# Kernel tuning notes

Measured on AMD Instinct MI355X. Metric: run time of the kernel, lower is better.

The kernel has to match this reference:

```python
import jax, jax.numpy as jnp
import numpy as np

H, KV, HD = 16, 8, 128           # heads, kv heads, head_dim
THETA, EPS = 1.0e6, 1e-6         # rope theta, rmsnorm eps
QMAX = 127.0                     # symmetric int8


def qdq(x):
    """Symmetric int8 fake quant-dequant along last dim (per-token / per-out-channel)."""
    s = jnp.maximum(jnp.max(jnp.abs(x), axis=-1, keepdims=True) / QMAX, 1e-8)
    q = jnp.clip(jnp.round(x / s), -QMAX, QMAX) * s
    return x + jax.lax.stop_gradient(q - x)  # STE


def rms_norm(x, w):
    v = jnp.mean(jnp.square(x.astype(jnp.float32)), axis=-1, keepdims=True)
    return (x.astype(jnp.float32) * jax.lax.rsqrt(v + EPS)).astype(x.dtype) * w


def rotate_half(x):
    x1, x2 = jnp.split(x, 2, axis=-1)
    return jnp.concatenate([-x2, x1], axis=-1)


def setup_inputs() -> dict:
    key = jax.random.key(0)
    ks = jax.random.split(key, 6)
    B, S, D = 1, 2048, 2048
    return {
        "hidden_states": jax.random.normal(ks[0], (B, S, D), jnp.float32),
        "Wq": jax.random.normal(ks[1], (H * HD, D), jnp.float32) * 0.02,
        "Wk": jax.random.normal(ks[2], (KV * HD, D), jnp.float32) * 0.02,
        "Wv": jax.random.normal(ks[3], (KV * HD, D), jnp.float32) * 0.02,
        "Wo": jax.random.normal(ks[4], (D, H * HD), jnp.float32) * 0.02,
        "q_norm_w": jnp.ones((HD,), jnp.float32),
        "k_norm_w": jnp.ones((HD,), jnp.float32),
        "position_ids": jnp.arange(S, dtype=jnp.int32)[None, :],
    }


def reference(hidden_states, Wq, Wk, Wv, Wo, q_norm_w, k_norm_w, position_ids):
    B, S, D = hidden_states.shape
    xq = qdq(hidden_states)                                  # per-token act quant (shared input)
    q = (xq @ qdq(Wq).T).reshape(B, S, H, HD).transpose(0, 2, 1, 3)   # [B,H,S,hd]
    k = (xq @ qdq(Wk).T).reshape(B, S, KV, HD).transpose(0, 2, 1, 3)  # [B,KV,S,hd]
    v = (xq @ qdq(Wv).T).reshape(B, S, KV, HD).transpose(0, 2, 1, 3)

    q = rms_norm(q, q_norm_w)
    k = rms_norm(k, k_norm_w)

    # rotary embeddings
    inv = 1.0 / (THETA ** (jnp.arange(0, HD, 2, dtype=jnp.float32) / HD))
    freqs = position_ids.astype(jnp.float32)[..., None] * inv          # [B,S,hd/2]
    emb = jnp.concatenate([freqs, freqs], axis=-1)                     # [B,S,hd]
    cos = jnp.cos(emb)[:, None].astype(q.dtype)                        # [B,1,S,hd]
    sin = jnp.sin(emb)[:, None].astype(q.dtype)
    q = q * cos + rotate_half(q) * sin
    k = k * cos + rotate_half(k) * sin

    # qkt_matmul.quant_x1 / quant_x2
    q = qdq(q)
    k = qdq(k)

    # GQA repeat
    g = H // KV
    k = jnp.repeat(k, g, axis=1)
    v = jnp.repeat(v, g, axis=1)

    scores = jnp.einsum("bhqd,bhkd->bhqk", q, k) * (HD ** -0.5)       # [B,H,S,S]
    causal = jnp.tril(jnp.ones((S, S), bool))
    scores = jnp.where(causal[None, None], scores, jnp.float32(-1e9))
    p = jax.nn.softmax(scores.astype(jnp.float32), axis=-1).astype(q.dtype)

    # pv_matmul.quant_x1 / quant_x2
    p = qdq(p)
    v = qdq(v)
    attn = jnp.einsum("bhqk,bhkd->bhqd", p, v)                        # [B,H,S,hd]
    attn = attn.transpose(0, 2, 1, 3).reshape(B, S, H * HD)
    return qdq(attn) @ qdq(Wo).T
```

## Files before the change

kernel.cpp:

```cpp
#include <hip/hip_runtime.h>
#include <math.h>

#define NH 16
#define NKV 8
#define HDIM 128
#define SEQ 2048
#define DMODEL 2048

typedef int   v4i __attribute__((ext_vector_type(4)));
typedef float v4f __attribute__((ext_vector_type(4)));
typedef _Float16 v8h __attribute__((ext_vector_type(8)));

static constexpr float SM_SCALE = 0.08838834764831843f;

#define GLOBP(p) (__attribute__((address_space(1))) void*)(p)
#define LDSP(p)  (__attribute__((address_space(3))) void*)(p)
#define ASYNC16(g, l) __builtin_amdgcn_global_load_lds(GLOBP(g), LDSP(l), 16, 0, 0)


__device__ __forceinline__ unsigned short f2h_bits(float x) {
    _Float16 h = (_Float16)x;
    return __builtin_bit_cast(unsigned short, h);
}

__global__ __launch_bounds__(256) void quant_all_k(const float* __restrict__ hidden,
        const float* __restrict__ Wq, const float* __restrict__ Wk,
        const float* __restrict__ Wv, const float* __restrict__ Wo,
        signed char* __restrict__ out, float* __restrict__ scale) {
    int p = blockIdx.x;
    int row0g = p * 16;
    const float* in; int lr0;
    if (row0g < 2048)      { in = hidden; lr0 = row0g; }
    else if (row0g < 4096) { in = Wq; lr0 = row0g - 2048; }
    else if (row0g < 5120) { in = Wk; lr0 = row0g - 4096; }
    else if (row0g < 6144) { in = Wv; lr0 = row0g - 5120; }
    else                   { in = Wo; lr0 = row0g - 6144; }
    const int cols = 2048;
    int tid = threadIdx.x;
    __shared__ float srow[16];
    int r = tid >> 4, l16 = tid & 15;
    const float4* x4 = (const float4*)(in + (size_t)(lr0 + r) * cols);
    float amax = 0.f;
    for (int c4 = l16; c4 < (cols >> 2); c4 += 16) {
        float4 v = x4[c4];
        amax = fmaxf(amax, fmaxf(fmaxf(fabsf(v.x), fabsf(v.y)),
                                 fmaxf(fabsf(v.z), fabsf(v.w))));
    }
#pragma unroll
    for (int m = 1; m <= 8; m <<= 1) amax = fmaxf(amax, __shfl_xor(amax, m));
    if (l16 == 0) {
        float s = fmaxf(amax / 127.0f, 1e-8f);
        srow[r] = s;
        scale[row0g + r] = s;
    }
    __syncthreads();
    int total = (cols >> 4) * 16;
    size_t obase = (size_t)p * 32768;
    for (int idx = tid; idx < total; idx += 256) {
        int f = idx >> 6, q = (idx >> 4) & 3, rr = idx & 15;
        const float* src = in + (size_t)(lr0 + rr) * cols + f * 64 + q * 16;
        float s = srow[rr];
        unsigned int wds[4];
#pragma unroll
        for (int g = 0; g < 4; ++g) {
            float4 v = *(const float4*)(src + g * 4);
            int b0 = (int)fminf(fmaxf(rintf(v.x / s), -127.f), 127.f);
            int b1 = (int)fminf(fmaxf(rintf(v.y / s), -127.f), 127.f);
            int b2 = (int)fminf(fmaxf(rintf(v.z / s), -127.f), 127.f);
            int b3 = (int)fminf(fmaxf(rintf(v.w / s), -127.f), 127.f);
            wds[g] = (b0 & 255) | ((b1 & 255) << 8) | ((b2 & 255) << 16) | ((b3 & 255) << 24);
        }
        *(uint4*)(out + obase + (size_t)idx * 16) =
            make_uint4(wds[0], wds[1], wds[2], wds[3]);
    }
}

__global__ __launch_bounds__(256) void row_quant_k(const float* __restrict__ in,
        signed char* __restrict__ out, float* __restrict__ scale, int cols) {
    int row0 = blockIdx.x * 16;
    int tid = threadIdx.x;
    __shared__ float srow[16];
    int r = tid >> 4, l16 = tid & 15;
    const float4* x4 = (const float4*)(in + (size_t)(row0 + r) * cols);
    float amax = 0.f;
    for (int c4 = l16; c4 < (cols >> 2); c4 += 16) {
        float4 v = x4[c4];
        amax = fmaxf(amax, fmaxf(fmaxf(fabsf(v.x), fabsf(v.y)),
                                 fmaxf(fabsf(v.z), fabsf(v.w))));
    }
#pragma unroll
    for (int m = 1; m <= 8; m <<= 1) amax = fmaxf(amax, __shfl_xor(amax, m));
    if (l16 == 0) {
        float s = fmaxf(amax / 127.0f, 1e-8f);
        srow[r] = s;
        scale[row0 + r] = s;
    }
    __syncthreads();
    int total = (cols >> 4) * 16;
    size_t obase = ((size_t)(row0 >> 4) * (cols >> 6)) << 10;
    for (int idx = tid; idx < total; idx += 256) {
        int f = idx >> 6, q = (idx >> 4) & 3, rr = idx & 15;
        const float* src = in + (size_t)(row0 + rr) * cols + f * 64 + q * 16;
        float s = srow[rr];
        unsigned int wds[4];
#pragma unroll
        for (int g = 0; g < 4; ++g) {
            float4 v = *(const float4*)(src + g * 4);
            int b0 = (int)fminf(fmaxf(rintf(v.x / s), -127.f), 127.f);
            int b1 = (int)fminf(fmaxf(rintf(v.y / s), -127.f), 127.f);
            int b2 = (int)fminf(fmaxf(rintf(v.z / s), -127.f), 127.f);
            int b3 = (int)fminf(fmaxf(rintf(v.w / s), -127.f), 127.f);
            wds[g] = (b0 & 255) | ((b1 & 255) << 8) | ((b2 & 255) << 16) | ((b3 & 255) << 24);
        }
        *(uint4*)(out + obase + (size_t)idx * 16) =
            make_uint4(wds[0], wds[1], wds[2], wds[3]);
    }
}

__global__ __launch_bounds__(256, 3) void gemm_i8_k(const signed char* __restrict__ A,
        const float* __restrict__ sa, const signed char* __restrict__ B,
        const float* __restrict__ sb, float* __restrict__ C, int M, int N, int K) {
    __shared__ __align__(16) signed char lsA[3][8192];
    __shared__ __align__(16) signed char lsB[3][8192];
    int tid = threadIdx.x;
    int w = tid >> 6, l = tid & 63;
    int wr = w >> 1, wc = w & 1;
    int lrow = l & 15;
    int m0 = blockIdx.y * 128, n0 = blockIdx.x * 128;
    int kb6 = K >> 6;
    v4i acc[4][4];
#pragma unroll
    for (int i = 0; i < 4; ++i)
#pragma unroll
        for (int j = 0; j < 4; ++j) acc[i][j] = (v4i){0, 0, 0, 0};

    auto stage = [&](int buf, int k6) {
#pragma unroll
        for (int a = 0; a < 2; ++a) {
            int f = a * 4 + w;
            ASYNC16(A + (((size_t)(((m0 >> 4) + f) * kb6 + k6)) << 10) + l * 16,
                    lsA[buf] + f * 1024);
            ASYNC16(B + (((size_t)(((n0 >> 4) + f) * kb6 + k6)) << 10) + l * 16,
                    lsB[buf] + f * 1024);
        }
    };

    stage(0, 0);
    if (kb6 > 1) {
        stage(1, 1);
        asm volatile("s_waitcnt vmcnt(4)" ::: "memory");
    } else {
        asm volatile("s_waitcnt vmcnt(0)" ::: "memory");
    }
    __builtin_amdgcn_s_barrier();
    for (int t = 0; t < kb6; ++t) {
        if (t + 2 < kb6) stage((t + 2) % 3, t + 2);
        int cur = t % 3;
        v4i af[4], bf[4];
#pragma unroll
        for (int i = 0; i < 4; ++i) af[i] = *(const v4i*)(lsA[cur] + (wr * 4 + i) * 1024 + l * 16);
#pragma unroll
        for (int j = 0; j < 4; ++j) bf[j] = *(const v4i*)(lsB[cur] + (wc * 4 + j) * 1024 + l * 16);
#pragma unroll
        for (int i = 0; i < 4; ++i)
#pragma unroll
            for (int j = 0; j < 4; ++j)
                acc[i][j] = __builtin_amdgcn_mfma_i32_16x16x64_i8(af[i], bf[j], acc[i][j], 0, 0, 0);
        if (t + 2 < kb6) asm volatile("s_waitcnt vmcnt(4)" ::: "memory");
        else             asm volatile("s_waitcnt vmcnt(0)" ::: "memory");
        __builtin_amdgcn_s_barrier();
    }
    int r0 = m0 + wr * 64, c0 = n0 + wc * 64;
    int lg = l >> 4;
    float sbv[4];
#pragma unroll
    for (int j = 0; j < 4; ++j) sbv[j] = sb[c0 + j * 16 + lrow];
#pragma unroll
    for (int i = 0; i < 4; ++i) {
        float4 s4 = *(const float4*)(sa + r0 + i * 16 + lg * 4);
        float sav[4] = {s4.x, s4.y, s4.z, s4.w};
#pragma unroll
        for (int j = 0; j < 4; ++j) {
#pragma unroll
            for (int reg = 0; reg < 4; ++reg) {
                int rr = r0 + i * 16 + lg * 4 + reg;
                C[(size_t)rr * N + c0 + j * 16 + lrow] = (float)acc[i][j][reg] * (sav[reg] * sbv[j]);
            }
        }
    }
}

__global__ __launch_bounds__(256, 2) void gemm_qkv_k(const signed char* __restrict__ A,
        const float* __restrict__ sa, const signed char* __restrict__ B,
        const float* __restrict__ sb,
        const float* __restrict__ qw, const float* __restrict__ kw,
        const float* __restrict__ ct, const float* __restrict__ st,
        signed char* __restrict__ q_i8, float* __restrict__ sq,
        signed char* __restrict__ k_i8, float* __restrict__ sk,
        unsigned short* __restrict__ vtT) {
    __shared__ __align__(16) char smem[68608];
    signed char (*lsA)[8192] = (signed char(*)[8192])smem;
    signed char (*lsB)[8192] = (signed char(*)[8192])(smem + 24576);
    float (*tile)[132] = (float(*)[132])smem;
    float* srow = (float*)(smem + 67584);
    int tid = threadIdx.x;
    int w = tid >> 6, l = tid & 63;
    int wr = w >> 1, wc = w & 1;
    int lrow = l & 15, lg = l >> 4;
    int m0 = blockIdx.y * 128, n0 = blockIdx.x * 128;
    const int kb6 = 32;
    v4i acc[4][4];
#pragma unroll
    for (int i = 0; i < 4; ++i)
#pragma unroll
        for (int j = 0; j < 4; ++j) acc[i][j] = (v4i){0, 0, 0, 0};

    auto stage = [&](int buf, int k6) {
#pragma unroll
        for (int a = 0; a < 2; ++a) {
            int f = a * 4 + w;
            ASYNC16(A + (((size_t)(((m0 >> 4) + f) * kb6 + k6)) << 10) + l * 16,
                    lsA[buf] + f * 1024);
            ASYNC16(B + (((size_t)(((n0 >> 4) + f) * kb6 + k6)) << 10) + l * 16,
                    lsB[buf] + f * 1024);
        }
    };

    stage(0, 0);
    stage(1, 1);
    asm volatile("s_waitcnt vmcnt(4)" ::: "memory");
    __builtin_amdgcn_s_barrier();
    for (int t = 0; t < kb6; ++t) {
        if (t + 2 < kb6) stage((t + 2) % 3, t + 2);
        int cur = t % 3;
        v4i af[4], bf[4];
#pragma unroll
        for (int i = 0; i < 4; ++i) af[i] = *(const v4i*)(lsA[cur] + (wr * 4 + i) * 1024 + l * 16);
#pragma unroll
        for (int j = 0; j < 4; ++j) bf[j] = *(const v4i*)(lsB[cur] + (wc * 4 + j) * 1024 + l * 16);
#pragma unroll
        for (int i = 0; i < 4; ++i)
#pragma unroll
            for (int j = 0; j < 4; ++j)
                acc[i][j] = __builtin_amdgcn_mfma_i32_16x16x64_i8(af[i], bf[j], acc[i][j], 0, 0, 0);
        if (t + 2 < kb6) asm volatile("s_waitcnt vmcnt(4)" ::: "memory");
        else             asm volatile("s_waitcnt vmcnt(0)" ::: "memory");
        __builtin_amdgcn_s_barrier();
    }
    {
        int c0 = n0 + wc * 64;
        float sbv[4];
#pragma unroll
        for (int j = 0; j < 4; ++j) sbv[j] = sb[c0 + j * 16 + lrow];
#pragma unroll
        for (int i = 0; i < 4; ++i) {
            float4 s4 = *(const float4*)(sa + m0 + wr * 64 + i * 16 + lg * 4);
            float sav[4] = {s4.x, s4.y, s4.z, s4.w};
#pragma unroll
            for (int j = 0; j < 4; ++j)
#pragma unroll
                for (int reg = 0; reg < 4; ++reg)
                    tile[wr * 64 + i * 16 + lg * 4 + reg][wc * 64 + j * 16 + lrow] =
                        (float)acc[i][j][reg] * (sav[reg] * sbv[j]);
        }
    }
    __syncthreads();
    int slot = n0 >> 7;
    if (slot < 24) {
        const float* wn = (slot < 16) ? qw : kw;
        signed char* dst8 = (slot < 16) ? q_i8 + (size_t)slot * (SEQ * 128)
                                        : k_i8 + (size_t)(slot - 16) * (SEQ * 128);
        float* sdst = (slot < 16) ? sq + (size_t)slot * SEQ : sk + (size_t)(slot - 16) * SEQ;
        float wn0 = wn[l], wn1 = wn[l + 64];
        for (int it = 0; it < 32; ++it) {
            int tl = it * 4 + w;
            int t = m0 + tl;
            float x0 = tile[tl][l];
            float x1 = tile[tl][l + 64];
            float ss = x0 * x0 + x1 * x1;
#pragma unroll
            for (int m = 1; m <= 32; m <<= 1) ss += __shfl_xor(ss, m);
            float rs = 1.0f / sqrtf(ss / 128.0f + 1e-6f);
            x0 = (x0 * rs) * wn0;
            x1 = (x1 * rs) * wn1;
            float cth = ct[t * 64 + l];
            float sth = st[t * 64 + l];
            float nx0 = x0 * cth - x1 * sth;
            float nx1 = x1 * cth + x0 * sth;
            float amax = fmaxf(fabsf(nx0), fabsf(nx1));
#pragma unroll
            for (int m = 1; m <= 32; m <<= 1) amax = fmaxf(amax, __shfl_xor(amax, m));
            float s = fmaxf(amax / 127.0f, 1e-8f);
            float q0 = fminf(fmaxf(rintf(nx0 / s), -127.f), 127.f);
            float q1 = fminf(fmaxf(rintf(nx1 / s), -127.f), 127.f);
            size_t ta0 = (size_t)(((t >> 4) * 2) << 10)
                       + (size_t)((((l >> 4) & 3) << 8) + ((t & 15) << 4) + (l & 15));
            dst8[ta0] = (signed char)(int)q0;
            dst8[ta0 + 1024] = (signed char)(int)q1;
            if (l == 0) sdst[t] = s;
        }
    } else {
        int kv = slot - 24;
        for (int it = 0; it < 32; ++it) {
            int tl = it * 4 + w;
            float x0 = tile[tl][l];
            float x1 = tile[tl][l + 64];
            float amax = fmaxf(fabsf(x0), fabsf(x1));
#pragma unroll
            for (int m = 1; m <= 32; m <<= 1) amax = fmaxf(amax, __shfl_xor(amax, m));
            if (l == 0) srow[tl] = fmaxf(amax / 127.0f, 1e-8f);
        }
        __syncthreads();
        int d = tid >> 1, th = (tid & 1) * 32;
        size_t base = (size_t)kv * (SEQ * 128);
#pragma unroll
        for (int kbl = 0; kbl < 2; ++kbl) {
            int kb = (m0 >> 6) + kbl;
#pragma unroll
            for (int j = 0; j < 32; j += 2) {
                int t64 = th + j;
                int tg = kbl * 64 + t64;
                float s0 = srow[tg], s1 = srow[tg + 1];
                float a = fminf(fmaxf(rintf(tile[tg][d] / s0), -127.f), 127.f) * s0;
                float b = fminf(fmaxf(rintf(tile[tg + 1][d] / s1), -127.f), 127.f) * s1;
                unsigned int ua = f2h_bits(a), ub = f2h_bits(b);
                int off = kb * 8192 + ((d >> 4) * 2 + ((t64 >> 5) & 1)) * 512
                        + (((d & 15) + (((t64 >> 3) & 3) << 4)) << 3) + (t64 & 7);
                *(unsigned int*)(vtT + base + off) = ua | (ub << 16);
            }
        }
    }
}

__global__ void rope_tab_k(const int* __restrict__ pos_ids,
                           float* __restrict__ ct, float* __restrict__ st) {
    int t = blockIdx.x;
    int fi = threadIdx.x;
    float inv = 1.0f / (float)pow(1.0e6, (double)fi / 64.0);
    float fr = (float)pos_ids[t] * inv;
    float sn, c;
    sincosf(fr, &sn, &c);
    ct[t * 64 + fi] = c;
    st[t * 64 + fi] = sn;
}

__global__ __launch_bounds__(256, 4) void attn_p1_k(const signed char* __restrict__ q_i8,
        const float* __restrict__ sq, const signed char* __restrict__ k_i8,
        const float* __restrict__ sk, float* __restrict__ mm) {
    int bx = blockIdx.x, hp = blockIdx.y;
    int qb = 31 - (bx >> 2), c = bx & 3;
    int nch = (qb + 8) >> 3;
    if (c >= nch) return;
    int q0 = qb * 64;
    int kb0 = c * 8, kb1 = min((c + 1) * 8, qb + 1);
    int tid = threadIdx.x, w = tid >> 6, l = tid & 63;
    int lrow = l & 15, lg = l >> 4;
    int h0 = hp * 2, h1 = h0 + 1;

    const signed char* qtA = q_i8 + (size_t)h0 * (SEQ * 128)
                           + ((size_t)((((q0 >> 4) + w) * 2)) << 10) + l * 16;
    const signed char* qtB = qtA + (size_t)(SEQ * 128);
    v4i qfA0 = *(const v4i*)(qtA), qfA1 = *(const v4i*)(qtA + 1024);
    v4i qfB0 = *(const v4i*)(qtB), qfB1 = *(const v4i*)(qtB + 1024);
    float4 sA = *(const float4*)(sq + (size_t)h0 * SEQ + q0 + w * 16 + lg * 4);
    float4 sB = *(const float4*)(sq + (size_t)h1 * SEQ + q0 + w * 16 + lg * 4);
    float sqrA[4] = {sA.x, sA.y, sA.z, sA.w};
    float sqrB[4] = {sB.x, sB.y, sB.z, sB.w};
    const signed char* kbase = k_i8 + (size_t)hp * (SEQ * 128);
    const float* skb = sk + (size_t)hp * SEQ;

    float mA[4], mB[4];
#pragma unroll
    for (int r = 0; r < 4; ++r) { mA[r] = -1e30f; mB[r] = -1e30f; }

    v4i ka[8], kn[8];
    float skc[4], skn[4];
    auto loadK = [&](v4i* dst, float* sdst, int k0) {
#pragma unroll
        for (int f = 0; f < 8; ++f)
            dst[f] = *(const v4i*)(kbase + ((size_t)((k0 >> 4) * 2 + f) << 10) + l * 16);
#pragma unroll
        for (int j = 0; j < 4; ++j) sdst[j] = skb[k0 + j * 16 + lrow];
    };

    loadK(ka, skc, kb0 * 64);
    for (int kb = kb0; kb < kb1; ++kb) {
        if (kb + 1 < kb1) loadK(kn, skn, (kb + 1) * 64);
        int k0 = kb * 64;
        v4i sciA[4], sciB[4];
#pragma unroll
        for (int j = 0; j < 4; ++j) {
            v4i z = {0, 0, 0, 0};
            v4i tA = __builtin_amdgcn_mfma_i32_16x16x64_i8(qfA0, ka[j * 2], z, 0, 0, 0);
            sciA[j] = __builtin_amdgcn_mfma_i32_16x16x64_i8(qfA1, ka[j * 2 + 1], tA, 0, 0, 0);
            v4i tB = __builtin_amdgcn_mfma_i32_16x16x64_i8(qfB0, ka[j * 2], z, 0, 0, 0);
            sciB[j] = __builtin_amdgcn_mfma_i32_16x16x64_i8(qfB1, ka[j * 2 + 1], tB, 0, 0, 0);
        }
#pragma unroll
        for (int reg = 0; reg < 4; ++reg) {
            int r = q0 + w * 16 + lg * 4 + reg;
#pragma unroll
            for (int j = 0; j < 4; ++j) {
                bool ok = (k0 + j * 16 + lrow <= r);
                float ss = skc[j] * SM_SCALE;
                float svA = ((float)sciA[j][reg] * sqrA[reg]) * ss;
                float svB = ((float)sciB[j][reg] * sqrB[reg]) * ss;
                mA[reg] = fmaxf(mA[reg], ok ? svA : -1e30f);
                mB[reg] = fmaxf(mB[reg], ok ? svB : -1e30f);
            }
        }
        if (kb + 1 < kb1) {
#pragma unroll
            for (int f = 0; f < 8; ++f) ka[f] = kn[f];
#pragma unroll
            for (int j = 0; j < 4; ++j) skc[j] = skn[j];
        }
    }
#pragma unroll
    for (int reg = 0; reg < 4; ++reg) {
#pragma unroll
        for (int mask = 1; mask <= 8; mask <<= 1) {
            mA[reg] = fmaxf(mA[reg], __shfl_xor(mA[reg], mask));
            mB[reg] = fmaxf(mB[reg], __shfl_xor(mB[reg], mask));
        }
    }
    if (lrow == 0) {
        size_t bA = ((size_t)(h0 * 32 + qb) * 4 + c) * 64;
        size_t bB = ((size_t)(h1 * 32 + qb) * 4 + c) * 64;
#pragma unroll
        for (int reg = 0; reg < 4; ++reg) {
            mm[bA + w * 16 + lg * 4 + reg] = mA[reg];
            mm[bB + w * 16 + lg * 4 + reg] = mB[reg];
        }
    }
}

__global__ __launch_bounds__(256, 2) void attn_p2_k(const signed char* __restrict__ q_i8,
        const float* __restrict__ sq, const signed char* __restrict__ k_i8,
        const float* __restrict__ sk, const unsigned short* __restrict__ vtT,
        const float* __restrict__ mm, float* __restrict__ attn2, float* __restrict__ pp,
        float* __restrict__ zb) {
    __shared__ __align__(16) unsigned short vlds[3][8192];
    __shared__ __align__(16) signed char klds[2][8192];
    __shared__ __align__(16) unsigned short plds[4096];
    __shared__ __align__(16) float slds[1024];
    int bx = blockIdx.x, hp = blockIdx.y;
    int qb = 31 - (bx >> 1), c = bx & 1;
    int nch2 = (qb >= 16) ? 2 : 1;
    if (c >= nch2) return;
    int q0 = qb * 64;
    int kb0 = c * 16, kb1 = min((c + 1) * 16, qb + 1);
    int tid = threadIdx.x, w = tid >> 6, l = tid & 63;
    int lrow = l & 15, lg = l >> 4;
    int h0 = hp * 2, h1 = h0 + 1;

    const signed char* qtA = q_i8 + (size_t)h0 * (SEQ * 128)
                           + ((size_t)((((q0 >> 4) + w) * 2)) << 10) + l * 16;
    const signed char* qtB = qtA + (size_t)(SEQ * 128);
    v4i qfA0 = *(const v4i*)(qtA), qfA1 = *(const v4i*)(qtA + 1024);
    v4i qfB0 = *(const v4i*)(qtB), qfB1 = *(const v4i*)(qtB + 1024);
    float4 sA = *(const float4*)(sq + (size_t)h0 * SEQ + q0 + w * 16 + lg * 4);
    float4 sB = *(const float4*)(sq + (size_t)h1 * SEQ + q0 + w * 16 + lg * 4);
    float sqrA[4] = {sA.x, sA.y, sA.z, sA.w};
    float sqrB[4] = {sB.x, sB.y, sB.z, sB.w};

    int nch1 = (qb + 8) >> 3;
    float mfA[4], mfB[4];
#pragma unroll
    for (int reg = 0; reg < 4; ++reg) {
        int r = w * 16 + lg * 4 + reg;
        float MA = -1e30f, MB = -1e30f;
        for (int c1 = 0; c1 < nch1; ++c1) {
            MA = fmaxf(MA, mm[((size_t)(h0 * 32 + qb) * 4 + c1) * 64 + r]);
            MB = fmaxf(MB, mm[((size_t)(h1 * 32 + qb) * 4 + c1) * 64 + r]);
        }
        mfA[reg] = MA; mfB[reg] = MB;
    }

    const signed char* kbase = k_i8 + (size_t)hp * (SEQ * 128);
    const float* skb = sk + (size_t)hp * SEQ;
    const unsigned short* vt = vtT + (size_t)hp * (SEQ * 128);

    auto issueV = [&](int kb) {
        unsigned short* vb = &vlds[kb % 3][0];
#pragma unroll
        for (int a = 0; a < 4; ++a) {
            int fv = a * 4 + w;
            ASYNC16(vt + (size_t)kb * 8192 + fv * 512 + l * 8, vb + fv * 512);
        }
    };
    auto issueK = [&](int kb) {
        signed char* kbuf = &klds[kb & 1][0];
#pragma unroll
        for (int a = 0; a < 2; ++a) {
            int f = a * 4 + w;
            ASYNC16(kbase + ((size_t)(kb * 8 + f) << 10) + l * 16, kbuf + f * 1024);
        }
    };

    v4f accA[8], accB[8];
#pragma unroll
    for (int jd = 0; jd < 8; ++jd) {
        accA[jd] = (v4f){0.f, 0.f, 0.f, 0.f};
        accB[jd] = (v4f){0.f, 0.f, 0.f, 0.f};
    }
    float ztA[4] = {0.f, 0.f, 0.f, 0.f};
    float ztB[4] = {0.f, 0.f, 0.f, 0.f};

    ASYNC16(skb + kb0 * 64 + w * 256 + l * 4, (char*)slds + w * 1024);
    issueK(kb0);
    issueV(kb0);
    if (kb0 + 1 < kb1) {
        issueV(kb0 + 1);
        asm volatile("s_waitcnt vmcnt(4)" ::: "memory");
    } else {
        asm volatile("s_waitcnt vmcnt(0)" ::: "memory");
    }
    __builtin_amdgcn_s_barrier();

    for (int kb = kb0; kb < kb1; ++kb) {
        int k0 = kb * 64;
        if (kb + 1 < kb1) issueK(kb + 1);
        if (kb + 2 < kb1) issueV(kb + 2);
        v4i ka[8];
#pragma unroll
        for (int f = 0; f < 8; ++f)
            ka[f] = *(const v4i*)(&klds[kb & 1][0] + f * 1024 + l * 16);
        float skc[4];
#pragma unroll
        for (int j = 0; j < 4; ++j) skc[j] = slds[(kb - kb0) * 64 + j * 16 + lrow];
        v4i sciA[4], sciB[4];
#pragma unroll
        for (int j = 0; j < 4; ++j) {
            v4i z = {0, 0, 0, 0};
            v4i tA = __builtin_amdgcn_mfma_i32_16x16x64_i8(qfA0, ka[j * 2], z, 0, 0, 0);
            sciA[j] = __builtin_amdgcn_mfma_i32_16x16x64_i8(qfA1, ka[j * 2 + 1], tA, 0, 0, 0);
            v4i tB = __builtin_amdgcn_mfma_i32_16x16x64_i8(qfB0, ka[j * 2], z, 0, 0, 0);
            sciB[j] = __builtin_amdgcn_mfma_i32_16x16x64_i8(qfB1, ka[j * 2 + 1], tB, 0, 0, 0);
        }
#pragma unroll
        for (int reg = 0; reg < 4; ++reg) {
            int rq = lg * 4 + reg;
            int r = q0 + w * 16 + rq;
#pragma unroll
            for (int j = 0; j < 4; ++j) {
                int cc = j * 16 + lrow;
                float pd = 0.f;
                if (k0 + cc <= r) {
                    float sv = ((float)sciA[j][reg] * (sqrA[reg] * skc[j])) * SM_SCALE;
                    float e = __expf(sv - mfA[reg]);
                    ztA[reg] += e;
                    pd = fminf(rintf(127.0f * e), 127.f);
                }
                plds[(w * 2 + (cc >> 5)) * 512 + (rq + 16 * ((cc >> 3) & 3)) * 8 + (cc & 7)] =
                    f2h_bits(pd);
            }
        }
        v8h pfA0 = *(const v8h*)(plds + (w * 2 + 0) * 512 + l * 8);
        v8h pfA1 = *(const v8h*)(plds + (w * 2 + 1) * 512 + l * 8);
#pragma unroll
        for (int reg = 0; reg < 4; ++reg) {
            int rq = lg * 4 + reg;
            int r = q0 + w * 16 + rq;
#pragma unroll
            for (int j = 0; j < 4; ++j) {
                int cc = j * 16 + lrow;
                float pd = 0.f;
                if (k0 + cc <= r) {
                    float sv = ((float)sciB[j][reg] * (sqrB[reg] * skc[j])) * SM_SCALE;
                    float e = __expf(sv - mfB[reg]);
                    ztB[reg] += e;
                    pd = fminf(rintf(127.0f * e), 127.f);
                }
                plds[(w * 2 + (cc >> 5)) * 512 + (rq + 16 * ((cc >> 3) & 3)) * 8 + (cc & 7)] =
                    f2h_bits(pd);
            }
        }
        v8h pfB0 = *(const v8h*)(plds + (w * 2 + 0) * 512 + l * 8);
        v8h pfB1 = *(const v8h*)(plds + (w * 2 + 1) * 512 + l * 8);
        const unsigned short* vb = &vlds[kb % 3][0];
#pragma unroll
        for (int jd = 0; jd < 8; ++jd) {
            v8h vh0 = *(const v8h*)(vb + (jd * 2 + 0) * 512 + l * 8);
            v8h vh1 = *(const v8h*)(vb + (jd * 2 + 1) * 512 + l * 8);
            v4f tA = accA[jd];
            tA = __builtin_amdgcn_mfma_f32_16x16x32_f16(pfA0, vh0, tA, 0, 0, 0);
            tA = __builtin_amdgcn_mfma_f32_16x16x32_f16(pfA1, vh1, tA, 0, 0, 0);
            accA[jd] = tA;
            v4f tB = accB[jd];
            tB = __builtin_amdgcn_mfma_f32_16x16x32_f16(pfB0, vh0, tB, 0, 0, 0);
            tB = __builtin_amdgcn_mfma_f32_16x16x32_f16(pfB1, vh1, tB, 0, 0, 0);
            accB[jd] = tB;
        }
        if (kb + 2 < kb1) asm volatile("s_waitcnt vmcnt(4)" ::: "memory");
        else              asm volatile("s_waitcnt vmcnt(0)" ::: "memory");
        __builtin_amdgcn_s_barrier();
    }
#pragma unroll
    for (int reg = 0; reg < 4; ++reg) {
#pragma unroll
        for (int mask = 1; mask <= 8; mask <<= 1) {
            ztA[reg] += __shfl_xor(ztA[reg], mask);
            ztB[reg] += __shfl_xor(ztB[reg], mask);
        }
    }
    if (qb < 16) {
        float spA[4], spB[4];
#pragma unroll
        for (int reg = 0; reg < 4; ++reg) {
            spA[reg] = fmaxf((1.0f / ztA[reg]) / 127.0f, 1e-8f);
            spB[reg] = fmaxf((1.0f / ztB[reg]) / 127.0f, 1e-8f);
        }
#pragma unroll
        for (int jd = 0; jd < 8; ++jd)
#pragma unroll
            for (int reg = 0; reg < 4; ++reg) {
                int r = q0 + w * 16 + lg * 4 + reg;
                attn2[(size_t)r * DMODEL + h0 * HDIM + jd * 16 + lrow] = accA[jd][reg] * spA[reg];
                attn2[(size_t)r * DMODEL + h1 * HDIM + jd * 16 + lrow] = accB[jd][reg] * spB[reg];
            }
    } else {
        if (c == 0) {
#pragma unroll
            for (int jd = 0; jd < 8; ++jd)
#pragma unroll
                for (int reg = 0; reg < 4; ++reg) {
                    int r = q0 + w * 16 + lg * 4 + reg;
                    attn2[(size_t)r * DMODEL + h0 * HDIM + jd * 16 + lrow] = accA[jd][reg];
                    attn2[(size_t)r * DMODEL + h1 * HDIM + jd * 16 + lrow] = accB[jd][reg];
                }
        } else {
#pragma unroll
            for (int jd = 0; jd < 8; ++jd)
#pragma unroll
                for (int reg = 0; reg < 4; ++reg) {
                    int rr = w * 16 + lg * 4 + reg;
                    pp[(((size_t)h0 * 16 + (qb - 16)) * 64 + rr) * 128 + jd * 16 + lrow] = accA[jd][reg];
                    pp[(((size_t)h1 * 16 + (qb - 16)) * 64 + rr) * 128 + jd * 16 + lrow] = accB[jd][reg];
                }
        }
        if (lrow == 0) {
            size_t zA = (((size_t)h0 * 16 + (qb - 16)) * 2 + c) * 64;
            size_t zB = (((size_t)h1 * 16 + (qb - 16)) * 2 + c) * 64;
#pragma unroll
            for (int reg = 0; reg < 4; ++reg) {
                zb[zA + w * 16 + lg * 4 + reg] = ztA[reg];
                zb[zB + w * 16 + lg * 4 + reg] = ztB[reg];
            }
        }
    }
}

__global__ __launch_bounds__(256) void attn_red_k(float* __restrict__ attn2,
        const float* __restrict__ pp, const float* __restrict__ zb) {
    int t16 = blockIdx.x, h = blockIdx.y;
    int qb = t16 + 16;
    int tid = threadIdx.x;
    for (int e = tid; e < 2048; e += 256) {
        int i = (e * 4) >> 7, j = (e * 4) & 127;
        float z0 = zb[(((size_t)h * 16 + t16) * 2 + 0) * 64 + i];
        float z1 = zb[(((size_t)h * 16 + t16) * 2 + 1) * 64 + i];
        float zinv = 1.0f / (z0 + z1);
        float spv = fmaxf(zinv / 127.0f, 1e-8f);
        float4 p = *(const float4*)&pp[(((size_t)h * 16 + t16) * 64 + i) * 128 + j];
        float* d = &attn2[(size_t)(qb * 64 + i) * DMODEL + h * HDIM + j];
        float4 dv = *(float4*)d;
        dv.x = (dv.x + p.x) * spv; dv.y = (dv.y + p.y) * spv;
        dv.z = (dv.z + p.z) * spv; dv.w = (dv.w + p.w) * spv;
        *(float4*)d = dv;
    }
}

extern "C" void kernel_launch(void* const* d_in, const int* in_sizes, int n_in,
                              void* d_out, int out_size, void* d_ws, size_t ws_size,
                              hipStream_t stream) {
    (void)in_sizes; (void)n_in; (void)out_size; (void)ws_size;
    const float* hidden = (const float*)d_in[0];
    const float* Wq = (const float*)d_in[1];
    const float* Wk = (const float*)d_in[2];
    const float* Wv = (const float*)d_in[3];
    const float* Wo = (const float*)d_in[4];
    const float* qw = (const float*)d_in[5];
    const float* kw = (const float*)d_in[6];
    const int* pos = (const int*)d_in[7];
    float* out = (float*)d_out;
    char* ws = (char*)d_ws;

    const size_t MB = 1024 * 1024;
    signed char* x_i8  = (signed char*)(ws);
    signed char* wq_i8 = (signed char*)(ws + 4 * MB);
    signed char* wo_i8 = (signed char*)(ws + 12 * MB);
    signed char* q_i8  = (signed char*)(ws + 16 * MB);
    signed char* k_i8  = (signed char*)(ws + 20 * MB);
    float* sx  = (float*)(ws + 22 * MB);
    float* swq = sx + 2048;
    float* swo = sx + 6144;
    float* sq  = sx + 8192;
    float* sk  = sq + NH * SEQ;
    float* sa  = sk + NKV * SEQ;
    float* ct  = (float*)(ws + 22 * MB + 512 * 1024);
    float* st  = (float*)(ws + 22 * MB + 1024 * 1024);
    float* attn2 = (float*)(ws + 32 * MB);
    float* pp    = (float*)(ws + 48 * MB);
    unsigned short* vtT = (unsigned short*)(ws + 56 * MB);
    float* mm    = (float*)(ws + 60 * MB);
    float* zb    = (float*)(ws + 60 * MB + 512 * 1024);
    signed char* a_i8 = x_i8;

    rope_tab_k<<<2048, 64, 0, stream>>>(pos, ct, st);
    quant_all_k<<<512, 256, 0, stream>>>(hidden, Wq, Wk, Wv, Wo, x_i8, sx);

    gemm_qkv_k<<<dim3(32, 16), 256, 0, stream>>>(x_i8, sx, wq_i8, swq, qw, kw, ct, st,
                                                 q_i8, sq, k_i8, sk, vtT);

    attn_p1_k<<<dim3(128, 8), 256, 0, stream>>>(q_i8, sq, k_i8, sk, mm);
    attn_p2_k<<<dim3(64, 8), 256, 0, stream>>>(q_i8, sq, k_i8, sk, vtT, mm, attn2, pp, zb);
    attn_red_k<<<dim3(16, 16), 256, 0, stream>>>(attn2, pp, zb);

    row_quant_k<<<128, 256, 0, stream>>>(attn2, a_i8, sa, 2048);
    gemm_i8_k<<<dim3(16, 16), 256, 0, stream>>>(a_i8, sa, wo_i8, swo, out, 2048, 2048, 2048);
}
```

Baseline: 194.2 us.

## Fuse rope table into quant, fold attention reduce into row quant, narrow O-GEMM tiles

The rope sin/cos table computation moves into extra blocks of the weight/activation quant kernel, and the split-softmax correction pass (attn_red_k) is folded into the row-quant kernel, which reads the partial PV buffer and normalizers directly. This removes two launches and one read-modify-write pass over attn2. The output GEMM switches to 128x64 tiles, giving 512 blocks instead of 256 for better CU occupancy on the 2048x2048 problem. In exchange, the row-quant kernel reads pp twice (once for amax, once for quantization) and each block's B-tile reuse drops.

```diff
diff --git a/kernel.cpp b/kernel.cpp
--- a/kernel.cpp
+++ b/kernel.cpp
@@ -23,11 +23,24 @@
     return __builtin_bit_cast(unsigned short, h);
 }
 
-__global__ __launch_bounds__(256) void quant_all_k(const float* __restrict__ hidden,
+__global__ __launch_bounds__(256) void quant_rope_k(const float* __restrict__ hidden,
         const float* __restrict__ Wq, const float* __restrict__ Wk,
         const float* __restrict__ Wv, const float* __restrict__ Wo,
-        signed char* __restrict__ out, float* __restrict__ scale) {
+        const int* __restrict__ pos_ids,
+        signed char* __restrict__ out, float* __restrict__ scale,
+        float* __restrict__ ct, float* __restrict__ st) {
     int p = blockIdx.x;
+    if (p >= 512) {
+        int t = (p - 512) * 4 + (threadIdx.x >> 6);
+        int fi = threadIdx.x & 63;
+        float inv = 1.0f / (float)pow(1.0e6, (double)fi / 64.0);
+        float fr = (float)pos_ids[t] * inv;
+        float sn, c;
+        sincosf(fr, &sn, &c);
+        ct[t * 64 + fi] = c;
+        st[t * 64 + fi] = sn;
+        return;
+    }
     int row0g = p * 16;
     const float* in; int lr0;
     if (row0g < 2048)      { in = hidden; lr0 = row0g; }
@@ -75,16 +88,38 @@
     }
 }
 
-__global__ __launch_bounds__(256) void row_quant_k(const float* __restrict__ in,
-        signed char* __restrict__ out, float* __restrict__ scale, int cols) {
+__global__ __launch_bounds__(256) void row_quant_red_k(const float* __restrict__ attn2,
+        const float* __restrict__ pp, const float* __restrict__ zb,
+        signed char* __restrict__ out, float* __restrict__ scale) {
     int row0 = blockIdx.x * 16;
+    bool corr = (row0 >= 1024);
     int tid = threadIdx.x;
     __shared__ float srow[16];
+    __shared__ float spvt[16][17];
+    if (corr) {
+        int r = tid >> 4, h = tid & 15;
+        int row = row0 + r;
+        int t16 = (row >> 6) - 16, rr = row & 63;
+        float z0 = zb[(((size_t)h * 16 + t16) * 2 + 0) * 64 + rr];
+        float z1 = zb[(((size_t)h * 16 + t16) * 2 + 1) * 64 + rr];
+        spvt[r][h] = fmaxf((1.0f / (z0 + z1)) / 127.0f, 1e-8f);
+    }
+    __syncthreads();
     int r = tid >> 4, l16 = tid & 15;
-    const float4* x4 = (const float4*)(in + (size_t)(row0 + r) * cols);
+    int row = row0 + r;
+    const float4* x4 = (const float4*)(attn2 + (size_t)row * 2048);
+    size_t ppr = corr ? ((((size_t)(row >> 6) - 16) * 64 + (row & 63)) * 128) : 0;
     float amax = 0.f;
-    for (int c4 = l16; c4 < (cols >> 2); c4 += 16) {
+    for (int c4 = l16; c4 < 512; c4 += 16) {
         float4 v = x4[c4];
+        if (corr) {
+            int h = c4 >> 5;
+            int j = (c4 & 31) * 4;
+            float4 pv = *(const float4*)&pp[(size_t)h * 16 * 64 * 128 + ppr + j];
+            float s = spvt[r][h];
+            v.x = (v.x + pv.x) * s; v.y = (v.y + pv.y) * s;
+            v.z = (v.z + pv.z) * s; v.w = (v.w + pv.w) * s;
+        }
         amax = fmaxf(amax, fmaxf(fmaxf(fabsf(v.x), fabsf(v.y)),
                                  fmaxf(fabsf(v.z), fabsf(v.w))));
     }
@@ -96,16 +131,26 @@
         scale[row0 + r] = s;
     }
     __syncthreads();
-    int total = (cols >> 4) * 16;
-    size_t obase = ((size_t)(row0 >> 4) * (cols >> 6)) << 10;
-    for (int idx = tid; idx < total; idx += 256) {
-        int f = idx >> 6, q = (idx >> 4) & 3, rr = idx & 15;
-        const float* src = in + (size_t)(row0 + rr) * cols + f * 64 + q * 16;
-        float s = srow[rr];
+    size_t obase = ((size_t)(row0 >> 4) * 32) << 10;
+    for (int idx = tid; idx < 2048; idx += 256) {
+        int f = idx >> 6, q = (idx >> 4) & 3, rr16 = idx & 15;
+        int rowb = row0 + rr16;
+        int colb = f * 64 + q * 16;
+        const float* src = attn2 + (size_t)rowb * 2048 + colb;
+        float s = srow[rr16];
+        int h = f >> 1;
+        float sp = corr ? spvt[rr16][h] : 0.f;
+        size_t ppb = corr ? ((size_t)h * 16 * 64 * 128
+                     + (((size_t)(rowb >> 6) - 16) * 64 + (rowb & 63)) * 128 + (colb & 127)) : 0;
         unsigned int wds[4];
 #pragma unroll
         for (int g = 0; g < 4; ++g) {
             float4 v = *(const float4*)(src + g * 4);
+            if (corr) {
+                float4 pv = *(const float4*)&pp[ppb + g * 4];
+                v.x = (v.x + pv.x) * sp; v.y = (v.y + pv.y) * sp;
+                v.z = (v.z + pv.z) * sp; v.w = (v.w + pv.w) * sp;
+            }
             int b0 = (int)fminf(fmaxf(rintf(v.x / s), -127.f), 127.f);
             int b1 = (int)fminf(fmaxf(rintf(v.y / s), -127.f), 127.f);
             int b2 = (int)fminf(fmaxf(rintf(v.z / s), -127.f), 127.f);
@@ -117,22 +162,22 @@
     }
 }
 
-__global__ __launch_bounds__(256, 3) void gemm_i8_k(const signed char* __restrict__ A,
+__global__ __launch_bounds__(256, 3) void gemm_o_k(const signed char* __restrict__ A,
         const float* __restrict__ sa, const signed char* __restrict__ B,
         const float* __restrict__ sb, float* __restrict__ C, int M, int N, int K) {
     __shared__ __align__(16) signed char lsA[3][8192];
-    __shared__ __align__(16) signed char lsB[3][8192];
+    __shared__ __align__(16) signed char lsB[3][4096];
     int tid = threadIdx.x;
     int w = tid >> 6, l = tid & 63;
     int wr = w >> 1, wc = w & 1;
     int lrow = l & 15;
-    int m0 = blockIdx.y * 128, n0 = blockIdx.x * 128;
+    int m0 = blockIdx.y * 128, n0 = blockIdx.x * 64;
     int kb6 = K >> 6;
-    v4i acc[4][4];
+    v4i acc[4][2];
 #pragma unroll
     for (int i = 0; i < 4; ++i)
 #pragma unroll
-        for (int j = 0; j < 4; ++j) acc[i][j] = (v4i){0, 0, 0, 0};
+        for (int j = 0; j < 2; ++j) acc[i][j] = (v4i){0, 0, 0, 0};
 
     auto stage = [&](int buf, int k6) {
 #pragma unroll
@@ -140,15 +185,15 @@
             int f = a * 4 + w;
             ASYNC16(A + (((size_t)(((m0 >> 4) + f) * kb6 + k6)) << 10) + l * 16,
                     lsA[buf] + f * 1024);
-            ASYNC16(B + (((size_t)(((n0 >> 4) + f) * kb6 + k6)) << 10) + l * 16,
-                    lsB[buf] + f * 1024);
-        }
+        }
+        ASYNC16(B + (((size_t)(((n0 >> 4) + w) * kb6 + k6)) << 10) + l * 16,
+                lsB[buf] + w * 1024);
     };
 
     stage(0, 0);
     if (kb6 > 1) {
         stage(1, 1);
-        asm volatile("s_waitcnt vmcnt(4)" ::: "memory");
+        asm volatile("s_waitcnt vmcnt(3)" ::: "memory");
     } else {
         asm volatile("s_waitcnt vmcnt(0)" ::: "memory");
     }
@@ -156,31 +201,31 @@
     for (int t = 0; t < kb6; ++t) {
         if (t + 2 < kb6) stage((t + 2) % 3, t + 2);
         int cur = t % 3;
-        v4i af[4], bf[4];
+        v4i af[4], bf[2];
 #pragma unroll
         for (int i = 0; i < 4; ++i) af[i] = *(const v4i*)(lsA[cur] + (wr * 4 + i) * 1024 + l * 16);
 #pragma unroll
-        for (int j = 0; j < 4; ++j) bf[j] = *(const v4i*)(lsB[cur] + (wc * 4 + j) * 1024 + l * 16);
+        for (int j = 0; j < 2; ++j) bf[j] = *(const v4i*)(lsB[cur] + (wc * 2 + j) * 1024 + l * 16);
 #pragma unroll
         for (int i = 0; i < 4; ++i)
 #pragma unroll
-            for (int j = 0; j < 4; ++j)
+            for (int j = 0; j < 2; ++j)
                 acc[i][j] = __builtin_amdgcn_mfma_i32_16x16x64_i8(af[i], bf[j], acc[i][j], 0, 0, 0);
-        if (t + 2 < kb6) asm volatile("s_waitcnt vmcnt(4)" ::: "memory");
+        if (t + 2 < kb6) asm volatile("s_waitcnt vmcnt(3)" ::: "memory");
         else             asm volatile("s_waitcnt vmcnt(0)" ::: "memory");
         __builtin_amdgcn_s_barrier();
     }
-    int r0 = m0 + wr * 64, c0 = n0 + wc * 64;
+    int r0 = m0 + wr * 64, c0 = n0 + wc * 32;
     int lg = l >> 4;
-    float sbv[4];
-#pragma unroll
-    for (int j = 0; j < 4; ++j) sbv[j] = sb[c0 + j * 16 + lrow];
+    float sbv[2];
+#pragma unroll
+    for (int j = 0; j < 2; ++j) sbv[j] = sb[c0 + j * 16 + lrow];
 #pragma unroll
     for (int i = 0; i < 4; ++i) {
         float4 s4 = *(const float4*)(sa + r0 + i * 16 + lg * 4);
         float sav[4] = {s4.x, s4.y, s4.z, s4.w};
 #pragma unroll
-        for (int j = 0; j < 4; ++j) {
+        for (int j = 0; j < 2; ++j) {
 #pragma unroll
             for (int reg = 0; reg < 4; ++reg) {
                 int rr = r0 + i * 16 + lg * 4 + reg;
@@ -332,18 +377,6 @@
     }
 }
 
-__global__ void rope_tab_k(const int* __restrict__ pos_ids,
-                           float* __restrict__ ct, float* __restrict__ st) {
-    int t = blockIdx.x;
-    int fi = threadIdx.x;
-    float inv = 1.0f / (float)pow(1.0e6, (double)fi / 64.0);
-    float fr = (float)pos_ids[t] * inv;
-    float sn, c;
-    sincosf(fr, &sn, &c);
-    ct[t * 64 + fi] = c;
-    st[t * 64 + fi] = sn;
-}
-
 __global__ __launch_bounds__(256, 4) void attn_p1_k(const signed char* __restrict__ q_i8,
         const float* __restrict__ sq, const signed char* __restrict__ k_i8,
         const float* __restrict__ sk, float* __restrict__ mm) {
@@ -648,26 +681,6 @@
                 zb[zB + w * 16 + lg * 4 + reg] = ztB[reg];
             }
         }
-    }
-}
-
-__global__ __launch_bounds__(256) void attn_red_k(float* __restrict__ attn2,
-        const float* __restrict__ pp, const float* __restrict__ zb) {
-    int t16 = blockIdx.x, h = blockIdx.y;
-    int qb = t16 + 16;
-    int tid = threadIdx.x;
-    for (int e = tid; e < 2048; e += 256) {
-        int i = (e * 4) >> 7, j = (e * 4) & 127;
-        float z0 = zb[(((size_t)h * 16 + t16) * 2 + 0) * 64 + i];
-        float z1 = zb[(((size_t)h * 16 + t16) * 2 + 1) * 64 + i];
-        float zinv = 1.0f / (z0 + z1);
-        float spv = fmaxf(zinv / 127.0f, 1e-8f);
-        float4 p = *(const float4*)&pp[(((size_t)h * 16 + t16) * 64 + i) * 128 + j];
-        float* d = &attn2[(size_t)(qb * 64 + i) * DMODEL + h * HDIM + j];
-        float4 dv = *(float4*)d;
-        dv.x = (dv.x + p.x) * spv; dv.y = (dv.y + p.y) * spv;
-        dv.z = (dv.z + p.z) * spv; dv.w = (dv.w + p.w) * spv;
-        *(float4*)d = dv;
     }
 }
 
@@ -707,16 +720,14 @@
     float* zb    = (float*)(ws + 60 * MB + 512 * 1024);
     signed char* a_i8 = x_i8;
 
-    rope_tab_k<<<2048, 64, 0, stream>>>(pos, ct, st);
-    quant_all_k<<<512, 256, 0, stream>>>(hidden, Wq, Wk, Wv, Wo, x_i8, sx);
+    quant_rope_k<<<1024, 256, 0, stream>>>(hidden, Wq, Wk, Wv, Wo, pos, x_i8, sx, ct, st);
 
     gemm_qkv_k<<<dim3(32, 16), 256, 0, stream>>>(x_i8, sx, wq_i8, swq, qw, kw, ct, st,
                                                  q_i8, sq, k_i8, sk, vtT);
 
     attn_p1_k<<<dim3(128, 8), 256, 0, stream>>>(q_i8, sq, k_i8, sk, mm);
     attn_p2_k<<<dim3(64, 8), 256, 0, stream>>>(q_i8, sq, k_i8, sk, vtT, mm, attn2, pp, zb);
-    attn_red_k<<<dim3(16, 16), 256, 0, stream>>>(attn2, pp, zb);
-
-    row_quant_k<<<128, 256, 0, stream>>>(attn2, a_i8, sa, 2048);
-    gemm_i8_k<<<dim3(16, 16), 256, 0, stream>>>(a_i8, sa, wo_i8, swo, out, 2048, 2048, 2048);
+
+    row_quant_red_k<<<128, 256, 0, stream>>>(attn2, pp, zb, a_i8, sa);
+    gemm_o_k<<<dim3(32, 16), 256, 0, stream>>>(a_i8, sa, wo_i8, swo, out, 2048, 2048, 2048);
 }
```

New measurement: 190.4 us. Within noise of the previous version (-1.9%).
